# Performance work log

Hardware: AMD Instinct MI355X
Metric: run time of the kernel (lower is better)

## Reference

```python
import jax, jax.numpy as jnp
import numpy as np
from jax import lax

C = 128       # capacity
D = 64        # latent_dims
K = 512       # K_vecs
BETA = 0.25
DN = ('NCHW', 'OIHW', 'NCHW')


def conv(x, w, b, stride=2, pad=1):
    y = lax.conv_general_dilated(x, w, (stride, stride), ((pad, pad), (pad, pad)),
                                 dimension_numbers=DN)
    return y + b[None, :, None, None]


def conv_transpose(x, w, b, stride=2, pad=1, k=4):
    # PyTorch ConvTranspose2d weight is (Cin, Cout, kh, kw); emulate via
    # lhs-dilated conv with spatially flipped, IO-swapped kernel.
    w2 = jnp.flip(w, axis=(-2, -1)).transpose(1, 0, 2, 3)  # -> OIHW
    p = k - 1 - pad
    y = lax.conv_general_dilated(x, w2, (1, 1), ((p, p), (p, p)),
                                 lhs_dilation=(stride, stride), dimension_numbers=DN)
    return y + b[None, :, None, None]


def setup_inputs() -> dict:
    key = jax.random.key(0)
    ks = jax.random.split(key, 11)
    s = 0.05
    return {
        'x': jax.random.uniform(ks[0], (32, 1, 256, 256), dtype=jnp.float32),
        'enc_w1': jax.random.normal(ks[1], (C, 1, 4, 4), jnp.float32) * s,
        'enc_b1': jnp.zeros((C,), jnp.float32),
        'enc_w2': jax.random.normal(ks[2], (D, C, 4, 4), jnp.float32) * s,
        'enc_b2': jnp.zeros((D,), jnp.float32),
        'codebook': jax.random.normal(ks[3], (K, D), jnp.float32),
        'dec_w2': jax.random.normal(ks[4], (D, C, 4, 4), jnp.float32) * s,  # ConvT: (Cin,Cout,kh,kw)
        'dec_b2': jnp.zeros((C,), jnp.float32),
        'dec_w1': jax.random.normal(ks[5], (C, 1, 4, 4), jnp.float32) * s,
        'dec_b1': jnp.zeros((1,), jnp.float32),
    }


def reference(x, enc_w1, enc_b1, enc_w2, enc_b2, codebook, dec_w2, dec_b2, dec_w1, dec_b1):
    # ---- encoder ----
    h = jax.nn.relu(conv(x, enc_w1, enc_b1))
    z = jax.nn.relu(conv(h, enc_w2, enc_b2))          # [B, D, H/4, W/4]

    # ---- vector quantizer ----
    z_nhwc = jnp.transpose(z, (0, 2, 3, 1))           # [B, h, w, D]
    flat = z_nhwc.reshape(-1, D)                      # [N, D]
    # mean-over-D squared distance, expanded form (no NxKxD tensor)
    d = (jnp.sum(flat * flat, axis=1, keepdims=True)
         - 2.0 * flat @ codebook.T
         + jnp.sum(codebook * codebook, axis=1)[None, :]) / D   # [N, K]
    idx = jnp.argmin(d, axis=1)                       # [N]
    quantized = codebook[idx].reshape(z_nhwc.shape)   # [B, h, w, D]

    codebook_loss = jnp.mean((quantized - lax.stop_gradient(z_nhwc)) ** 2)
    commitment_loss = jnp.mean((lax.stop_gradient(quantized) - z_nhwc) ** 2)
    vq_loss = codebook_loss + BETA * commitment_loss

    # straight-through estimator (training mode)
    quantized_st = z_nhwc + lax.stop_gradient(quantized - z_nhwc)
    q_nchw = jnp.transpose(quantized_st, (0, 3, 1, 2))

    # ---- decoder ----
    g = jax.nn.relu(conv_transpose(q_nchw, dec_w2, dec_b2))
    x_recon = jax.nn.sigmoid(conv_transpose(g, dec_w1, dec_b1))

    return vq_loss, idx[:, None].astype(jnp.int32), x_recon
```

## Files before the change

kernel.cpp:

```cpp
#include <hip/hip_runtime.h>
#include <math.h>


#define REC_OFF 131073

typedef unsigned short ushort_t;
typedef __attribute__((ext_vector_type(8))) short bf16x8;
typedef __attribute__((ext_vector_type(4))) float f32x4;
typedef __attribute__((ext_vector_type(4))) unsigned int u32x4;
union FragU { u32x4 u; bf16x8 h; };

__device__ __forceinline__ unsigned pack_hilo(float v) {
  unsigned u = __float_as_uint(v);
  unsigned htop = u & 0xFFFF0000u;
  float rf = v - __uint_as_float(htop);
  return htop | (__float_as_uint(rf) >> 16);
}

__global__ __launch_bounds__(64) void zero_loss_k(float* __restrict__ out) {
  if (threadIdx.x == 0) out[0] = 0.f;
}

__global__ __launch_bounds__(256) void repackA2_k(
    const float* __restrict__ ew2,
    ushort_t* __restrict__ hi, ushort_t* __restrict__ lo) {
  int idx = blockIdx.x * 256 + threadIdx.x;
  int j = idx & 7, l = (idx >> 3) & 63, mt = (idx >> 9) & 3, ks = idx >> 11;
  int ci = ((ks >> 2) << 3) + ((l >> 4) << 1) + (j >> 2);
  int ky = ks & 3, kx = j & 3, d = (mt << 4) + (l & 15);
  float val = ew2[((d << 7) + ci) * 16 + (ky << 2) + kx];
  unsigned u = __float_as_uint(val);
  float rf = val - __uint_as_float(u & 0xFFFF0000u);
  hi[idx] = (ushort_t)(u >> 16);
  lo[idx] = (ushort_t)(__float_as_uint(rf) >> 16);
}

__global__ __launch_bounds__(256) void repackA_k(
    const float* __restrict__ dw2,
    ushort_t* __restrict__ hi, ushort_t* __restrict__ lo) {
  int idx = blockIdx.x * 256 + threadIdx.x;
  int j = idx & 7, l = (idx >> 3) & 63, mt = (idx >> 9) & 7;
  int s = (idx >> 12) & 7, v = idx >> 15;
  int co = (mt << 4) + (l & 15);
  int ci = (s << 3) + ((l >> 4) << 1) + (j >> 2);
  int tap = j & 3;
  int Yp = v >> 1, pX = v & 1;
  int kyA = 1 - Yp, kyB = kyA + 2;
  int kxA = pX ? 0 : 1, kxB = kxA + 2;
  int ky = (tap & 2) ? kyB : kyA;
  int kx = (tap & 1) ? kxA : kxB;
  float val = dw2[(((ci << 7) + co) << 4) + (ky << 2) + kx];
  unsigned u = __float_as_uint(val);
  float rf = val - __uint_as_float(u & 0xFFFF0000u);
  hi[idx] = (ushort_t)(u >> 16);
  lo[idx] = (ushort_t)(__float_as_uint(rf) >> 16);
}

__global__ __launch_bounds__(256) void repackCB_k(
    const float* __restrict__ cb,
    ushort_t* __restrict__ hi, ushort_t* __restrict__ lo) {
  int idx = blockIdx.x * 256 + threadIdx.x;
  int j = idx & 7, l = (idx >> 3) & 63, mt = (idx >> 9) & 31, ks = idx >> 14;
  int code = (mt << 4) + (l & 15);
  int k = (ks << 5) + ((l >> 4) << 3) + j;
  float val = cb[(code << 6) + k];
  unsigned u = __float_as_uint(val);
  float rf = val - __uint_as_float(u & 0xFFFF0000u);
  hi[idx] = (ushort_t)(u >> 16);
  lo[idx] = (ushort_t)(__float_as_uint(rf) >> 16);
}

__global__ __launch_bounds__(256) void csqF_k(
    const float* __restrict__ cb, float* __restrict__ csqF) {
  int idx = blockIdx.x * 256 + threadIdx.x;
  int r = idx & 3, l = (idx >> 2) & 63, mt = idx >> 8;
  int code = (mt << 4) + ((l >> 4) << 2) + r;
  const float* cp = cb + (code << 6);
  float s = 0.f;
#pragma unroll
  for (int d = 0; d < 64; ++d) s = fmaf(cp[d], cp[d], s);
  csqF[idx] = s;
}

__global__ __launch_bounds__(128) void conv1_k(
    const float* __restrict__ x, const float* __restrict__ w1,
    const float* __restrict__ b1, unsigned* __restrict__ hp) {
  int oy = blockIdx.x, b = blockIdx.y, ox = threadIdx.x;
  float xv[16];
#pragma unroll
  for (int ky = 0; ky < 4; ++ky) {
    int iy = 2 * oy - 1 + ky;
#pragma unroll
    for (int kx = 0; kx < 4; ++kx) {
      int ix = 2 * ox - 1 + kx;
      float v = 0.f;
      if (iy >= 0 && iy < 256 && ix >= 0 && ix < 256)
        v = x[(b * 256 + iy) * 256 + ix];
      xv[ky * 4 + kx] = v;
    }
  }
  for (int c = 0; c < 128; ++c) {
    const float* wp = w1 + c * 16;
    float acc = b1[c];
#pragma unroll
    for (int k = 0; k < 16; ++k) acc = fmaf(xv[k], wp[k], acc);
    hp[((b * 128 + c) * 128 + oy) * 128 + ox] = pack_hilo(fmaxf(acc, 0.f));
  }
}

#define C2RL 133
__global__ __launch_bounds__(256) void conv2_k(
    const unsigned* __restrict__ hp, const ushort_t* __restrict__ wCh,
    const ushort_t* __restrict__ wCl, const float* __restrict__ b2,
    float* __restrict__ z) {
  __shared__ unsigned hs[8][4][C2RL];
  int y = blockIdx.x, b = blockIdx.y;
  int t = threadIdx.x, l = t & 63;
  int w = __builtin_amdgcn_readfirstlane(t >> 6);
  int g = l >> 4;

  if (t < 64) hs[t >> 3][(t >> 1) & 3][(t & 1) ? 129 : 0] = 0u;

  int ci_l = t >> 5, l32 = t & 31;
  int iy[4];
  bool rowok[4];
#pragma unroll
  for (int r = 0; r < 4; ++r) {
    iy[r] = 2 * y - 1 + r;
    rowok[r] = iy[r] >= 0 && iy[r] < 128;
  }
  const unsigned* hbase = hp + (((long)b * 128) << 14);

  u32x4 pre[4];
#pragma unroll
  for (int r = 0; r < 4; ++r)
    pre[r] = rowok[r]
        ? *reinterpret_cast<const u32x4*>(
              hbase + (((long)ci_l << 14) + (iy[r] << 7)) + 4 * l32)
        : (u32x4)0u;

  f32x4 acc[4];
#pragma unroll
  for (int nt = 0; nt < 4; ++nt) acc[nt] = (f32x4)0.f;

  for (int rnd = 0; rnd < 16; ++rnd) {
    __syncthreads();
#pragma unroll
    for (int r = 0; r < 4; ++r) {
      unsigned* dst = &hs[ci_l][r][1 + 4 * l32];
      dst[0] = pre[r][0]; dst[1] = pre[r][1];
      dst[2] = pre[r][2]; dst[3] = pre[r][3];
    }
    __syncthreads();
    if (rnd < 15) {
      long cb8 = ((long)((rnd + 1) * 8 + ci_l)) << 14;
#pragma unroll
      for (int r = 0; r < 4; ++r)
        pre[r] = rowok[r]
            ? *reinterpret_cast<const u32x4*>(
                  hbase + cb8 + (iy[r] << 7) + 4 * l32)
            : (u32x4)0u;
    }
#pragma unroll
    for (int ky = 0; ky < 4; ++ky) {
      int ks = (rnd << 2) + ky;
      FragU ah, al_;
      long aoff = (((long)ks * 4 + w) * 64 + l) * 8;
      ah.u = *reinterpret_cast<const u32x4*>(wCh + aoff);
      al_.u = *reinterpret_cast<const u32x4*>(wCl + aoff);
#pragma unroll
      for (int nt = 0; nt < 4; ++nt) {
        const unsigned* pa = &hs[g * 2][ky][(nt << 5) + 2 * (l & 15)];
        const unsigned* pb = &hs[g * 2 + 1][ky][(nt << 5) + 2 * (l & 15)];
        unsigned a0 = pa[0], a1 = pa[1], a2 = pa[2], a3 = pa[3];
        unsigned b0 = pb[0], b1 = pb[1], b2_ = pb[2], b3 = pb[3];
        FragU bh, bl;
        bh.u[0] = __builtin_amdgcn_perm(a1, a0, 0x07060302u);
        bl.u[0] = __builtin_amdgcn_perm(a1, a0, 0x05040100u);
        bh.u[1] = __builtin_amdgcn_perm(a3, a2, 0x07060302u);
        bl.u[1] = __builtin_amdgcn_perm(a3, a2, 0x05040100u);
        bh.u[2] = __builtin_amdgcn_perm(b1, b0, 0x07060302u);
        bl.u[2] = __builtin_amdgcn_perm(b1, b0, 0x05040100u);
        bh.u[3] = __builtin_amdgcn_perm(b3, b2_, 0x07060302u);
        bl.u[3] = __builtin_amdgcn_perm(b3, b2_, 0x05040100u);
        acc[nt] = __builtin_amdgcn_mfma_f32_16x16x32_bf16(
            ah.h, bh.h, acc[nt], 0, 0, 0);
        acc[nt] = __builtin_amdgcn_mfma_f32_16x16x32_bf16(
            ah.h, bl.h, acc[nt], 0, 0, 0);
        acc[nt] = __builtin_amdgcn_mfma_f32_16x16x32_bf16(
            al_.h, bh.h, acc[nt], 0, 0, 0);
      }
    }
  }
#pragma unroll
  for (int nt = 0; nt < 4; ++nt) {
#pragma unroll
    for (int r = 0; r < 4; ++r) {
      int d = (w << 4) + (g << 2) + r;
      int x = (nt << 4) + (l & 15);
      float v = fmaxf(acc[nt][r] + b2[d], 0.f);
      z[((b * 64 + d) * 64 + y) * 64 + x] = v;
    }
  }
}

__global__ __launch_bounds__(256) void vq_k(
    const float* z, const float* __restrict__ cb,
    const ushort_t* __restrict__ cbFh, const ushort_t* __restrict__ cbFl,
    const float* __restrict__ csqF, unsigned int* q_pk,
    float* __restrict__ out, int n0) {
  __shared__ unsigned zS[64 * 67];
  __shared__ int bk_arr[64];
  __shared__ float redl[4];
  int t = threadIdx.x, l = t & 63;
  int w = __builtin_amdgcn_readfirstlane(t >> 6);
  int nbase = blockIdx.x * 64;
  int b = nbase >> 12, y = (nbase >> 6) & 63;
  long zbase = (long)b * 262144 + y * 64;

  float zv[16];
#pragma unroll
  for (int j = 0; j < 16; ++j) {
    zv[j] = z[zbase + (long)((w << 4) + j) * 4096 + l];
    zS[l * 67 + (w << 4) + j] = pack_hilo(zv[j]);
  }
  __syncthreads();

  int pp = (w << 4) + (l & 15);
  FragU bh[2], bl[2];
#pragma unroll
  for (int ks = 0; ks < 2; ++ks) {
    const unsigned* zp = &zS[pp * 67 + (ks << 5) + ((l >> 4) << 3)];
    unsigned u0 = zp[0], u1 = zp[1], u2 = zp[2], u3 = zp[3];
    unsigned u4 = zp[4], u5 = zp[5], u6 = zp[6], u7 = zp[7];
    bh[ks].u[0] = __builtin_amdgcn_perm(u1, u0, 0x07060302u);
    bl[ks].u[0] = __builtin_amdgcn_perm(u1, u0, 0x05040100u);
    bh[ks].u[1] = __builtin_amdgcn_perm(u3, u2, 0x07060302u);
    bl[ks].u[1] = __builtin_amdgcn_perm(u3, u2, 0x05040100u);
    bh[ks].u[2] = __builtin_amdgcn_perm(u5, u4, 0x07060302u);
    bl[ks].u[2] = __builtin_amdgcn_perm(u5, u4, 0x05040100u);
    bh[ks].u[3] = __builtin_amdgcn_perm(u7, u6, 0x07060302u);
    bl[ks].u[3] = __builtin_amdgcn_perm(u7, u6, 0x05040100u);
  }

  int g = l >> 4;
  float bd = 1e30f;
  int bk = 0;
  for (int mc = 0; mc < 4; ++mc) {
    f32x4 acc[8];
#pragma unroll
    for (int m8 = 0; m8 < 8; ++m8) acc[m8] = (f32x4)0.f;
#pragma unroll
    for (int ks = 0; ks < 2; ++ks) {
#pragma unroll
      for (int m8 = 0; m8 < 8; ++m8) {
        long aoff = (((long)(ks * 32 + mc * 8 + m8) * 64) + l) * 8;
        FragU ah, al_;
        ah.u = *reinterpret_cast<const u32x4*>(cbFh + aoff);
        al_.u = *reinterpret_cast<const u32x4*>(cbFl + aoff);
        acc[m8] = __builtin_amdgcn_mfma_f32_16x16x32_bf16(
            ah.h, bh[ks].h, acc[m8], 0, 0, 0);
        acc[m8] = __builtin_amdgcn_mfma_f32_16x16x32_bf16(
            ah.h, bl[ks].h, acc[m8], 0, 0, 0);
        acc[m8] = __builtin_amdgcn_mfma_f32_16x16x32_bf16(
            al_.h, bh[ks].h, acc[m8], 0, 0, 0);
      }
    }
#pragma unroll
    for (int m8 = 0; m8 < 8; ++m8) {
      int mt = mc * 8 + m8;
      f32x4 cq = *reinterpret_cast<const f32x4*>(csqF + ((mt << 6) + l) * 4);
#pragma unroll
      for (int r = 0; r < 4; ++r) {
        float d = fmaf(-2.f, acc[m8][r], cq[r]);
        if (d < bd) { bd = d; bk = (mt << 4) + (g << 2) + r; }
      }
    }
  }
#pragma unroll
  for (int m = 16; m <= 32; m <<= 1) {
    float d2 = __shfl_xor(bd, m);
    int k2 = __shfl_xor(bk, m);
    if (d2 < bd || (d2 == bd && k2 < bk)) { bd = d2; bk = k2; }
  }
  if (l < 16) {
    bk_arr[(w << 4) + l] = bk;
    out[1 + n0 + nbase + (w << 4) + l] = (float)bk;
  }
  __syncthreads();

  int bkp = bk_arr[l];
  const float* cbest = cb + (bkp << 6) + (w << 4);
  float ls = 0.f;
#pragma unroll
  for (int j = 0; j < 16; ++j) {
    float c = cbest[j];
    q_pk[zbase + (long)((w << 4) + j) * 4096 + l] = pack_hilo(c);
    float df = c - zv[j];
    ls = fmaf(df, df, ls);
  }
#pragma unroll
  for (int m = 32; m; m >>= 1) ls += __shfl_xor(ls, m);
  if (l == 0) redl[w] = ls;
  __syncthreads();
  if (t == 0)
    atomicAdd(out, (redl[0] + redl[1] + redl[2] + redl[3]) * (1.25f / 8388608.f));
}

__global__ __launch_bounds__(512) void dconv2_k(
    const unsigned int* __restrict__ q_pk, const ushort_t* __restrict__ wAh,
    const ushort_t* __restrict__ wAl, const float* __restrict__ db2,
    float* __restrict__ g) {
  __shared__ unsigned int rows[64][3][68];
  int a = blockIdx.x, b = blockIdx.y;
  int t = threadIdx.x, l = t & 63;
  int w = __builtin_amdgcn_readfirstlane(t >> 6);
  int Yloc = w >> 2, pX = w & 1, coh = (w >> 1) & 1;
  int Y = 2 * a + Yloc;
  int v = (Yloc << 1) | pX;
  int rA = Yloc + 1, rB = Yloc;

  if (t < 192) {
    int ci = t & 63, r = t >> 6;
    rows[ci][r][0] = 0u;
    rows[ci][r][65] = 0u;
  }
  long qb = (long)b * 262144;
#pragma unroll
  for (int r = 0; r < 3; ++r) {
    int yr = a - 1 + r;
    bool ok = (yr >= 0) && (yr < 64);
    for (int s = t; s < 1024; s += 512) {
      int ci = s >> 4, c4 = s & 15;
      u32x4 val = ok ? *reinterpret_cast<const u32x4*>(
                           q_pk + qb + ci * 4096 + yr * 64 + (c4 << 2))
                     : (u32x4)0u;
      unsigned* dst = &rows[ci][r][1 + (c4 << 2)];
      dst[0] = val[0]; dst[1] = val[1]; dst[2] = val[2]; dst[3] = val[3];
    }
  }
  __syncthreads();

  f32x4 acc[4][4];
#pragma unroll
  for (int mt = 0; mt < 4; ++mt)
#pragma unroll
    for (int nt = 0; nt < 4; ++nt) acc[mt][nt] = (f32x4)0.f;

  for (int s8 = 0; s8 < 8; ++s8) {
    FragU ah[4], al[4];
#pragma unroll
    for (int mt = 0; mt < 4; ++mt) {
      long off = ((((long)(v * 8 + s8) * 8 + (coh * 4 + mt)) * 64 + l) * 8);
      ah[mt].u = *reinterpret_cast<const u32x4*>(wAh + off);
      al[mt].u = *reinterpret_cast<const u32x4*>(wAl + off);
    }
#pragma unroll
    for (int nt = 0; nt < 4; ++nt) {
      int p = nt * 16 + (l & 15) + pX;
      int cc0 = (s8 << 3) + ((l >> 4) << 1);
      unsigned u0 = rows[cc0][rA][p], u1 = rows[cc0][rA][p + 1];
      unsigned u2 = rows[cc0][rB][p], u3 = rows[cc0][rB][p + 1];
      unsigned u4 = rows[cc0 + 1][rA][p], u5 = rows[cc0 + 1][rA][p + 1];
      unsigned u6 = rows[cc0 + 1][rB][p], u7 = rows[cc0 + 1][rB][p + 1];
      FragU bh, bl;
      bh.u[0] = (u0 >> 16) | (u1 & 0xFFFF0000u);
      bl.u[0] = (u0 & 0xFFFFu) | (u1 << 16);
      bh.u[1] = (u2 >> 16) | (u3 & 0xFFFF0000u);
      bl.u[1] = (u2 & 0xFFFFu) | (u3 << 16);
      bh.u[2] = (u4 >> 16) | (u5 & 0xFFFF0000u);
      bl.u[2] = (u4 & 0xFFFFu) | (u5 << 16);
      bh.u[3] = (u6 >> 16) | (u7 & 0xFFFF0000u);
      bl.u[3] = (u6 & 0xFFFFu) | (u7 << 16);
#pragma unroll
      for (int mt = 0; mt < 4; ++mt) {
        acc[mt][nt] = __builtin_amdgcn_mfma_f32_16x16x32_bf16(
            ah[mt].h, bh.h, acc[mt][nt], 0, 0, 0);
        acc[mt][nt] = __builtin_amdgcn_mfma_f32_16x16x32_bf16(
            ah[mt].h, bl.h, acc[mt][nt], 0, 0, 0);
        acc[mt][nt] = __builtin_amdgcn_mfma_f32_16x16x32_bf16(
            al[mt].h, bh.h, acc[mt][nt], 0, 0, 0);
      }
    }
  }

#pragma unroll
  for (int mt = 0; mt < 4; ++mt) {
#pragma unroll
    for (int r = 0; r < 4; ++r) {
      int co = ((coh * 4 + mt) << 4) + ((l >> 4) << 2) + r;
      float bias = db2[co];
#pragma unroll
      for (int nt = 0; nt < 4; ++nt) {
        int X = ((nt << 4) + (l & 15)) * 2 + pX;
        float val = fmaxf(acc[mt][nt][r] + bias, 0.f);
        g[((b * 128 + co) * 128 + Y) * 128 + X] = val;
      }
    }
  }
}

__global__ __launch_bounds__(256) void dconv1_k(
    const float* __restrict__ g, const float* __restrict__ wd1,
    const float* __restrict__ db1, float* __restrict__ rec) {
  int a2 = blockIdx.x, b = blockIdx.y;
  int t = threadIdx.x;
  int w = __builtin_amdgcn_readfirstlane(t >> 6);
  int l = t & 63;
  int xh = w >> 1, pX = w & 1;
  int L = xh * 64 + l;
  int kxA = pX ? 0 : 1, kxB = kxA + 2;
  int ixH = L + pX, ixL = L + pX - 1;
  bool okH = ixH < 128, okL = ixL >= 0;
  int yy0 = 2 * a2 - 1;
  bool vy[4];
#pragma unroll
  for (int r = 0; r < 4; ++r) vy[r] = (yy0 + r) >= 0 && (yy0 + r) < 128;

  const float* gb = g + ((long)b * 128) * 16384 + (long)yy0 * 128;
  float acc[4] = {0.f, 0.f, 0.f, 0.f};

  for (int ci = 0; ci < 128; ci += 2) {
    const float* p0 = gb + (long)ci * 16384;
    const float* p1 = p0 + 16384;
    float hi0[4], lo0[4], hi1[4], lo1[4];
#pragma unroll
    for (int r = 0; r < 4; ++r) {
      const float* q0 = p0 + r * 128;
      const float* q1 = p1 + r * 128;
      hi0[r] = (vy[r] && okH) ? q0[ixH] : 0.f;
      lo0[r] = (vy[r] && okL) ? q0[ixL] : 0.f;
      hi1[r] = (vy[r] && okH) ? q1[ixH] : 0.f;
      lo1[r] = (vy[r] && okL) ? q1[ixL] : 0.f;
    }
    const float* wp0 = wd1 + ci * 16;
    const float* wp1 = wp0 + 16;
#pragma unroll
    for (int j = 0; j < 4; ++j) {
      int kyA = (j + 1) & 1, kyB = kyA + 2;
      int rA = ((j + 1) >> 1) + 1;
      float v = acc[j];
      v = fmaf(wp0[kyA * 4 + kxA], hi0[rA], v);
      v = fmaf(wp0[kyA * 4 + kxB], lo0[rA], v);
      v = fmaf(wp0[kyB * 4 + kxA], hi0[rA - 1], v);
      v = fmaf(wp0[kyB * 4 + kxB], lo0[rA - 1], v);
      v = fmaf(wp1[kyA * 4 + kxA], hi1[rA], v);
      v = fmaf(wp1[kyA * 4 + kxB], lo1[rA], v);
      v = fmaf(wp1[kyB * 4 + kxA], hi1[rA - 1], v);
      v = fmaf(wp1[kyB * 4 + kxB], lo1[rA - 1], v);
      acc[j] = v;
    }
  }
  float bb = db1[0];
#pragma unroll
  for (int j = 0; j < 4; ++j) {
    float v = acc[j] + bb;
    v = 1.f / (1.f + __expf(-v));
    rec[((b * 256 + 4 * a2 + j) * 256) + 2 * L + pX] = v;
  }
}

extern "C" void kernel_launch(void* const* d_in, const int* in_sizes, int n_in,
                              void* d_out, int out_size, void* d_ws, size_t ws_size,
                              hipStream_t stream) {
  const float* x      = (const float*)d_in[0];
  const float* enc_w1 = (const float*)d_in[1];
  const float* enc_b1 = (const float*)d_in[2];
  const float* enc_w2 = (const float*)d_in[3];
  const float* enc_b2 = (const float*)d_in[4];
  const float* cb     = (const float*)d_in[5];
  const float* dec_w2 = (const float*)d_in[6];
  const float* dec_b2 = (const float*)d_in[7];
  const float* dec_w1 = (const float*)d_in[8];
  const float* dec_b1 = (const float*)d_in[9];

  float* out = (float*)d_out;
  float* ws  = (float*)d_ws;
  ushort_t* wCh  = (ushort_t*)ws;
  ushort_t* wCl  = (ushort_t*)(ws + 65536);
  ushort_t* wAh  = (ushort_t*)(ws + 131072);
  ushort_t* wAl  = (ushort_t*)(ws + 196608);
  ushort_t* cbFh = (ushort_t*)(ws + 262144);
  ushort_t* cbFl = (ushort_t*)(ws + 278528);
  float* csqF = ws + 294912;
  float* dyn  = ws + 303104;

  const size_t PER_IMG = 2097152 + 262144;
  size_t avail = (ws_size / 4 > 303104 + 64) ? ws_size / 4 - 303104 - 64 : 0;
  int CB = 32;
  while (CB > 1 && (size_t)CB * PER_IMG > avail) CB >>= 1;

  zero_loss_k<<<dim3(1), 64, 0, stream>>>(out);
  repackA2_k<<<dim3(512), 256, 0, stream>>>(enc_w2, wCh, wCl);
  repackA_k<<<dim3(512), 256, 0, stream>>>(dec_w2, wAh, wAl);
  repackCB_k<<<dim3(128), 256, 0, stream>>>(cb, cbFh, cbFl);
  csqF_k<<<dim3(32), 256, 0, stream>>>(cb, csqF);

  for (int b0 = 0; b0 < 32; b0 += CB) {
    unsigned* hp = (unsigned*)dyn;
    float* zq = dyn + (size_t)CB * 2097152;
    conv1_k<<<dim3(128, CB), 128, 0, stream>>>(
        x + (size_t)b0 * 65536, enc_w1, enc_b1, hp);
    conv2_k<<<dim3(64, CB), 256, 0, stream>>>(hp, wCh, wCl, enc_b2, zq);
    vq_k<<<dim3(CB * 64), 256, 0, stream>>>(
        zq, cb, cbFh, cbFl, csqF, (unsigned int*)zq, out, b0 * 4096);
    dconv2_k<<<dim3(64, CB), 512, 0, stream>>>(
        (const unsigned int*)zq, wAh, wAl, dec_b2, (float*)dyn );
    dconv1_k<<<dim3(64, CB), 256, 0, stream>>>(
        (float*)dyn , dec_w1, dec_b1, out + REC_OFF + (size_t)b0 * 65536);
  }
}
```

Baseline: 561.5 us.

## Compute two output rows per conv2 block to share overlapping input rows

The encoder conv2 kernel now uses 512-thread blocks, each producing two adjacent output rows. The two rows share a 6-row input halo staged in LDS, where the old 256-thread blocks each loaded 4 rows for one output row. This cuts global reads of the hidden activation by about a quarter and halves the grid size. The cost is more LDS per block and fewer blocks, which may reduce occupancy and latency hiding.

Result: no change. 568.1 us (+1.2%).

```diff
diff --git a/kernel.cpp b/kernel.cpp
--- a/kernel.cpp
+++ b/kernel.cpp
@@ -109,34 +109,40 @@
 }
 
 #define C2RL 133
-__global__ __launch_bounds__(256) void conv2_k(
+__global__ __launch_bounds__(512) void conv2_k(
     const unsigned* __restrict__ hp, const ushort_t* __restrict__ wCh,
     const ushort_t* __restrict__ wCl, const float* __restrict__ b2,
     float* __restrict__ z) {
-  __shared__ unsigned hs[8][4][C2RL];
-  int y = blockIdx.x, b = blockIdx.y;
+  __shared__ unsigned hs[8][6][C2RL];
+  int a = blockIdx.x, b = blockIdx.y;
   int t = threadIdx.x, l = t & 63;
   int w = __builtin_amdgcn_readfirstlane(t >> 6);
+  int Yloc = w >> 2, mt = w & 3;
+  int y = 2 * a + Yloc;
   int g = l >> 4;
 
-  if (t < 64) hs[t >> 3][(t >> 1) & 3][(t & 1) ? 129 : 0] = 0u;
-
-  int ci_l = t >> 5, l32 = t & 31;
-  int iy[4];
-  bool rowok[4];
-#pragma unroll
-  for (int r = 0; r < 4; ++r) {
-    iy[r] = 2 * y - 1 + r;
-    rowok[r] = iy[r] >= 0 && iy[r] < 128;
+  if (t < 48) {
+    int ci = t & 7, r = t >> 3;
+    hs[ci][r][0] = 0u;
+    hs[ci][r][129] = 0u;
+  }
+
+  int c4 = t & 31, ci_l = (t >> 5) & 7, r0 = t >> 8;
+  int yr[3];
+  bool rowok[3];
+#pragma unroll
+  for (int i = 0; i < 3; ++i) {
+    yr[i] = 4 * a - 1 + r0 + 2 * i;
+    rowok[i] = yr[i] >= 0 && yr[i] < 128;
   }
   const unsigned* hbase = hp + (((long)b * 128) << 14);
 
-  u32x4 pre[4];
-#pragma unroll
-  for (int r = 0; r < 4; ++r)
-    pre[r] = rowok[r]
+  u32x4 pre[3];
+#pragma unroll
+  for (int i = 0; i < 3; ++i)
+    pre[i] = rowok[i]
         ? *reinterpret_cast<const u32x4*>(
-              hbase + (((long)ci_l << 14) + (iy[r] << 7)) + 4 * l32)
+              hbase + (((long)ci_l << 14) + (yr[i] << 7)) + (c4 << 2))
         : (u32x4)0u;
 
   f32x4 acc[4];
@@ -146,32 +152,33 @@
   for (int rnd = 0; rnd < 16; ++rnd) {
     __syncthreads();
 #pragma unroll
-    for (int r = 0; r < 4; ++r) {
-      unsigned* dst = &hs[ci_l][r][1 + 4 * l32];
-      dst[0] = pre[r][0]; dst[1] = pre[r][1];
-      dst[2] = pre[r][2]; dst[3] = pre[r][3];
+    for (int i = 0; i < 3; ++i) {
+      unsigned* dst = &hs[ci_l][r0 + 2 * i][1 + (c4 << 2)];
+      dst[0] = pre[i][0]; dst[1] = pre[i][1];
+      dst[2] = pre[i][2]; dst[3] = pre[i][3];
     }
     __syncthreads();
     if (rnd < 15) {
       long cb8 = ((long)((rnd + 1) * 8 + ci_l)) << 14;
 #pragma unroll
-      for (int r = 0; r < 4; ++r)
-        pre[r] = rowok[r]
+      for (int i = 0; i < 3; ++i)
+        pre[i] = rowok[i]
             ? *reinterpret_cast<const u32x4*>(
-                  hbase + cb8 + (iy[r] << 7) + 4 * l32)
+                  hbase + cb8 + (yr[i] << 7) + (c4 << 2))
             : (u32x4)0u;
     }
 #pragma unroll
     for (int ky = 0; ky < 4; ++ky) {
       int ks = (rnd << 2) + ky;
+      int row = 2 * Yloc + ky;
       FragU ah, al_;
-      long aoff = (((long)ks * 4 + w) * 64 + l) * 8;
+      long aoff = (((long)ks * 4 + mt) * 64 + l) * 8;
       ah.u = *reinterpret_cast<const u32x4*>(wCh + aoff);
       al_.u = *reinterpret_cast<const u32x4*>(wCl + aoff);
 #pragma unroll
       for (int nt = 0; nt < 4; ++nt) {
-        const unsigned* pa = &hs[g * 2][ky][(nt << 5) + 2 * (l & 15)];
-        const unsigned* pb = &hs[g * 2 + 1][ky][(nt << 5) + 2 * (l & 15)];
+        const unsigned* pa = &hs[g * 2][row][(nt << 5) + 2 * (l & 15)];
+        const unsigned* pb = &hs[g * 2 + 1][row][(nt << 5) + 2 * (l & 15)];
         unsigned a0 = pa[0], a1 = pa[1], a2 = pa[2], a3 = pa[3];
         unsigned b0 = pb[0], b1 = pb[1], b2_ = pb[2], b3 = pb[3];
         FragU bh, bl;
@@ -196,7 +203,7 @@
   for (int nt = 0; nt < 4; ++nt) {
 #pragma unroll
     for (int r = 0; r < 4; ++r) {
-      int d = (w << 4) + (g << 2) + r;
+      int d = (mt << 4) + (g << 2) + r;
       int x = (nt << 4) + (l & 15);
       float v = fmaxf(acc[nt][r] + b2[d], 0.f);
       z[((b * 64 + d) * 64 + y) * 64 + x] = v;
@@ -501,7 +508,7 @@
     float* zq = dyn + (size_t)CB * 2097152;
     conv1_k<<<dim3(128, CB), 128, 0, stream>>>(
         x + (size_t)b0 * 65536, enc_w1, enc_b1, hp);
-    conv2_k<<<dim3(64, CB), 256, 0, stream>>>(hp, wCh, wCl, enc_b2, zq);
+    conv2_k<<<dim3(32, CB), 512, 0, stream>>>(hp, wCh, wCl, enc_b2, zq);
     vq_k<<<dim3(CB * 64), 256, 0, stream>>>(
         zq, cb, cbFh, cbFl, csqF, (unsigned int*)zq, out, b0 * 4096);
     dconv2_k<<<dim3(64, CB), 512, 0, stream>>>(
```
